# Kernel tuning notes

Measured on AMD Instinct MI355X. Metric: run time of the kernel, lower is better.

Reference implementation:

```python
import jax, jax.numpy as jnp
import numpy as np

IMG = 800.0        # image size (square)
STRIDE = 16        # backbone stride
PRE = 6000         # pre-NMS proposals (test_before_rpn_proposal_num)
POST = 300         # post-NMS proposals (test_after_rpn_proposal_num)
OUT = 7            # RoIAlign output size
SR = 2             # sampling ratio (fixed stand-in for adaptive -1)
NMS_THR = 0.7      # rpn_nms_thr_iou
MIN_SIZE = 16.0    # rpn_min_size
NCLS = 21          # num_classes + background
NEG = -1e30


def xywh2xyxy(b):
    return jnp.concatenate([b[..., :2], b[..., :2] + b[..., 2:]], -1)


def iou_one_vs_all(box, boxes):
    x1 = jnp.maximum(box[0], boxes[:, 0]); y1 = jnp.maximum(box[1], boxes[:, 1])
    x2 = jnp.minimum(box[2], boxes[:, 2]); y2 = jnp.minimum(box[3], boxes[:, 3])
    inter = jnp.maximum(x2 - x1, 0.0) * jnp.maximum(y2 - y1, 0.0)
    a = (box[2] - box[0]) * (box[3] - box[1])
    b = (boxes[:, 2] - boxes[:, 0]) * (boxes[:, 3] - boxes[:, 1])
    return inter / (a + b - inter + 1e-9)


def nms(boxes, scores, thr, k):
    # Greedy NMS with a fixed number of kept boxes (jit-static shapes).
    boxes = jax.lax.stop_gradient(boxes)
    scores = jax.lax.stop_gradient(scores)
    n = scores.shape[0]
    idx = jnp.arange(n)

    def step(sc, _):
        best = jnp.argmax(sc)
        ious = iou_one_vs_all(boxes[best], boxes)
        sc = jnp.where((ious > thr) | (idx == best), NEG, sc)
        return sc, best

    _, keep = jax.lax.scan(step, scores, None, length=k)
    return keep  # [k] int32 indices


def roi_align(feat, rois_xyxy, scale, out, sr):
    # feat [C,H,W], rois_xyxy [K,4] in image coords -> [K,C,out,out]
    C, H, W = feat.shape
    K = rois_xyxy.shape[0]
    x1 = rois_xyxy[:, 0] * scale; y1 = rois_xyxy[:, 1] * scale
    x2 = rois_xyxy[:, 2] * scale; y2 = rois_xyxy[:, 3] * scale
    bw = (x2 - x1) / out; bh = (y2 - y1) / out
    grid = jnp.arange(out, dtype=jnp.float32)
    sub = (jnp.arange(sr, dtype=jnp.float32) + 0.5) / sr
    xs = x1[:, None, None] + (grid[None, :, None] + sub[None, None, :]) * bw[:, None, None]  # [K,out,sr]
    ys = y1[:, None, None] + (grid[None, :, None] + sub[None, None, :]) * bh[:, None, None]
    shp = (K, out, out, sr, sr)  # [K, oy, ox, sy, sx]
    xg = jnp.broadcast_to(xs[:, None, :, None, :], shp)
    yg = jnp.broadcast_to(ys[:, :, None, :, None], shp)
    x0 = jnp.floor(xg); y0 = jnp.floor(yg)
    wx = xg - x0; wy = yg - y0
    x0i = jnp.clip(x0.astype(jnp.int32), 0, W - 1); x1i = jnp.clip(x0i + 1, 0, W - 1)
    y0i = jnp.clip(y0.astype(jnp.int32), 0, H - 1); y1i = jnp.clip(y0i + 1, 0, H - 1)
    v00 = feat[:, y0i, x0i]  # [C,K,out,out,sr,sr]
    v01 = feat[:, y0i, x1i]
    v10 = feat[:, y1i, x0i]
    v11 = feat[:, y1i, x1i]
    wx = wx[None]; wy = wy[None]
    val = v00 * (1 - wy) * (1 - wx) + v01 * (1 - wy) * wx + v10 * wy * (1 - wx) + v11 * wy * wx
    pooled = val.mean(axis=(-1, -2))  # [C,K,out,out]
    return jnp.transpose(pooled, (1, 0, 2, 3))


def _forward(feat, proposals, scores, fc1_w, fc1_b, fc2_w, fc2_b, cls_w, cls_b, reg_w, reg_b):
    std = jnp.tile(jnp.array([0.1, 0.1, 0.2, 0.2], jnp.float32), NCLS)  # target_std per class

    def per_image(fb, pr, sc):
        # mark small proposals as ignored (score -> -inf), as in forward
        sc = jnp.where((pr[:, 2] < MIN_SIZE) | (pr[:, 3] < MIN_SIZE), NEG, sc)
        tsc, tid = jax.lax.top_k(sc, PRE)
        tb = pr[tid]                       # [PRE,4] xywh
        txyxy = xywh2xyxy(tb)
        keep = nms(txyxy, tsc, NMS_THR, POST)
        sb = tb[keep]                      # [POST,4] xywh
        sxyxy = txyxy[keep]
        rf = roi_align(fb, sxyxy, 1.0 / STRIDE, OUT, SR)   # [POST,512,7,7]
        x = rf.reshape(POST, -1)
        x = jax.nn.relu(x @ fc1_w + fc1_b)
        x = jax.nn.relu(x @ fc2_w + fc2_b)
        cls = x @ cls_w + cls_b            # [POST,21]
        reg = (x @ reg_w + reg_b) * std    # reg * target_std + target_mean(=0)
        reg = reg.reshape(POST, NCLS, 4)
        # proposal2bbox: xy = p_xy + d_xy*p_wh ; wh = p_wh * exp(d_wh)
        xy = sb[:, None, :2] + reg[..., :2] * sb[:, None, 2:]
        wh = sb[:, None, 2:] * jnp.exp(reg[..., 2:])
        dec = jnp.clip(jnp.concatenate([xy, xy + wh], -1), 0.0, IMG)
        return jnp.concatenate([jax.nn.softmax(cls, -1), dec.reshape(POST, NCLS * 4)], -1)

    return jax.vmap(per_image)(feat, proposals, scores)  # [B, POST, 21 + 84]


def setup_inputs() -> dict:
    key = jax.random.key(0)
    ks = jax.random.split(key, 12)
    B, C, H, W = 1, 512, 50, 50
    N = 22500  # 50*50*9 anchors
    feat = jax.random.normal(ks[0], (B, C, H, W), jnp.float32)
    xy = jax.random.uniform(ks[1], (B, N, 2), jnp.float32) * (IMG - 64.0)
    wh = 8.0 + jax.random.uniform(ks[2], (B, N, 2), jnp.float32) * 392.0  # some below min_size=16
    proposals = jnp.concatenate([xy, wh], -1)
    scores = jax.random.uniform(ks[3], (B, N), jnp.float32)
    D = C * OUT * OUT  # 25088
    return {
        "feat": feat,
        "proposals": proposals,
        "scores": scores,
        "fc1_w": jax.random.normal(ks[4], (D, 4096), jnp.float32) * 0.01,
        "fc1_b": jnp.zeros((4096,), jnp.float32),
        "fc2_w": jax.random.normal(ks[5], (4096, 4096), jnp.float32) * 0.01,
        "fc2_b": jnp.zeros((4096,), jnp.float32),
        "cls_w": jax.random.normal(ks[6], (4096, NCLS), jnp.float32) * 0.01,
        "cls_b": jnp.zeros((NCLS,), jnp.float32),
        "reg_w": jax.random.normal(ks[7], (4096, NCLS * 4), jnp.float32) * 0.001,
        "reg_b": jnp.zeros((NCLS * 4,), jnp.float32),
    }


def reference(feat, proposals, scores, fc1_w, fc1_b, fc2_w, fc2_b, cls_w, cls_b, reg_w, reg_b):
    return _forward(feat, proposals, scores, fc1_w, fc1_b, fc2_w, fc2_b, cls_w, cls_b, reg_w, reg_b)
```

## Files before the change

### kernel.cpp

```cpp
#include <hip/hip_runtime.h>
#include <stdint.h>


#define NEGV -1e30f

typedef __attribute__((ext_vector_type(8))) short short8;
typedef __attribute__((ext_vector_type(4))) float f32x4;

__device__ __forceinline__ uint16_t f2bf(float f) {
  uint32_t u = __builtin_bit_cast(uint32_t, f);
  u = (u + 0x7FFFu + ((u >> 16) & 1u)) >> 16;
  return (uint16_t)u;
}
__device__ __forceinline__ float bf2f(uint16_t h) {
  return __builtin_bit_cast(float, ((uint32_t)h) << 16);
}
__device__ __forceinline__ uint32_t fkey(float f) {
  uint32_t u = __builtin_bit_cast(uint32_t, f);
  return (u & 0x80000000u) ? ~u : (u | 0x80000000u);
}

__global__ __launch_bounds__(256) void prep_kernel(
    const float* __restrict__ proposals, const float* __restrict__ scores,
    uint32_t* __restrict__ keys, uint64_t* __restrict__ sortbuf,
    int* __restrict__ counter) {
  int i = blockIdx.x * 256 + threadIdx.x;
  if (i < 8192) sortbuf[i] = 0ULL;
  if (i == 0) *counter = 0;
  if (i < 22500) {
    float w = proposals[i * 4 + 2], h = proposals[i * 4 + 3];
    float s = scores[i];
    s = (w < 16.0f || h < 16.0f) ? NEGV : s;
    keys[i] = fkey(s);
  }
}

__global__ __launch_bounds__(1024) void select_kernel(
    const uint32_t* __restrict__ keys, uint32_t* __restrict__ cutoff) {
  __shared__ uint32_t hist[256];
  __shared__ uint32_t s_prefix;
  __shared__ int s_remaining;
  int tid = threadIdx.x;
  if (tid == 0) { s_prefix = 0; s_remaining = 6000; }
  __syncthreads();
  for (int round = 0; round < 4; round++) {
    int shift = 24 - round * 8;
    for (int i = tid; i < 256; i += 1024) hist[i] = 0;
    __syncthreads();
    uint32_t prefix = s_prefix;
    uint32_t pmask = (round == 0) ? 0u : (0xFFFFFFFFu << (shift + 8));
    for (int i = tid; i < 22500; i += 1024) {
      uint32_t kv = keys[i];
      if ((kv & pmask) == (prefix & pmask))
        atomicAdd(&hist[(kv >> shift) & 255u], 1u);
    }
    __syncthreads();
    if (tid == 0) {
      int rem = s_remaining;
      int chosen = 0;
      for (int b = 255; b >= 0; b--) {
        int c = (int)hist[b];
        if (c >= rem) { chosen = b; break; }
        rem -= c;
      }
      s_prefix = prefix | ((uint32_t)chosen << shift);
      s_remaining = rem;
    }
    __syncthreads();
  }
  if (tid == 0) *cutoff = s_prefix;
}

__global__ __launch_bounds__(256) void compact_kernel(
    const uint32_t* __restrict__ keys, const uint32_t* __restrict__ cutoff,
    uint64_t* __restrict__ sortbuf, int* __restrict__ counter) {
  int i = blockIdx.x * 256 + threadIdx.x;
  if (i >= 22500) return;
  uint32_t kv = keys[i];
  if (kv >= *cutoff) {
    int p = atomicAdd(counter, 1);
    if (p < 8192)
      sortbuf[p] = ((uint64_t)kv << 32) | (uint32_t)(~(uint32_t)i);
  }
}

__global__ __launch_bounds__(1024) void sort_kernel(
    const uint64_t* __restrict__ sortbuf, int* __restrict__ sorted_idx) {
  __shared__ uint64_t v[8192];
  int tid = threadIdx.x;
  for (int i = tid; i < 8192; i += 1024) v[i] = sortbuf[i];
  __syncthreads();
  for (int k = 2; k <= 8192; k <<= 1) {
    for (int j = k >> 1; j > 0; j >>= 1) {
      for (int i = tid; i < 8192; i += 1024) {
        int ixj = i ^ j;
        if (ixj > i) {
          uint64_t a = v[i], b = v[ixj];
          bool up = (i & k) == 0;
          if (up ? (a < b) : (a > b)) { v[i] = b; v[ixj] = a; }
        }
      }
      __syncthreads();
    }
  }
  for (int i = tid; i < 6000; i += 1024)
    sorted_idx[i] = (int)(~(uint32_t)(v[i] & 0xFFFFFFFFull));
}

__global__ __launch_bounds__(256) void gather_kernel(
    const float* __restrict__ proposals, const int* __restrict__ sorted_idx,
    float4* __restrict__ sxyxy, float4* __restrict__ sxywh) {
  int i = blockIdx.x * 256 + threadIdx.x;
  if (i >= 6000) return;
  int oi = sorted_idx[i];
  float x = proposals[oi * 4 + 0], y = proposals[oi * 4 + 1];
  float w = proposals[oi * 4 + 2], h = proposals[oi * 4 + 3];
  sxywh[i] = make_float4(x, y, w, h);
  sxyxy[i] = make_float4(x, y, x + w, y + h);
}

__global__ __launch_bounds__(256) void ioumat_kernel(
    const float4* __restrict__ boxes, uint32_t* __restrict__ M) {
#pragma clang fp contract(off)
  int idx = blockIdx.x * 256 + threadIdx.x;
  if (idx >= 6000 * 188) return;
  int j = idx / 188;
  int w = idx - j * 188;
  float4 bb = boxes[j];
  float ba = (bb.z - bb.x) * (bb.w - bb.y);
  int base = w * 32;
  int lim = min(6000 - base, 32);
  uint32_t bits = 0;
  for (int b = 0; b < lim; b++) {
    float4 ob = boxes[base + b];
    float xx1 = fmaxf(bb.x, ob.x);
    float yy1 = fmaxf(bb.y, ob.y);
    float xx2 = fminf(bb.z, ob.z);
    float yy2 = fminf(bb.w, ob.w);
    float inter = fmaxf(xx2 - xx1, 0.0f) * fmaxf(yy2 - yy1, 0.0f);
    float oa = (ob.z - ob.x) * (ob.w - ob.y);
    float iou = inter / (ba + oa - inter + 1e-9f);
    if (iou > 0.7f) bits |= (1u << b);
  }
  M[idx] = bits;
}

__global__ __launch_bounds__(256) void nms_reduce_kernel(
    const uint32_t* __restrict__ M, const float4* __restrict__ sxyxy,
    const float4* __restrict__ sxywh, float4* __restrict__ keep_xyxy,
    float4* __restrict__ keep_xywh) {
  __shared__ uint32_t remv[188];
  __shared__ int keeps[300];
  __shared__ int s_ck[64];
  __shared__ int s_nk, s_nck;
  int tid = threadIdx.x;
  if (tid < 188) remv[tid] = (tid == 187) ? 0xFFFF0000u : 0u;
  if (tid == 0) { s_nk = 0; s_nck = 0; }
  __syncthreads();
  for (int c = 0; c < 94; c++) {
    if (tid < 64) {
      int row = c * 64 + tid;
      uint32_t lo = 0, hi = 0;
      if (row < 6000) {
        lo = M[(size_t)row * 188 + 2 * c];
        hi = M[(size_t)row * 188 + 2 * c + 1];
      }
      uint64_t alive =
          ~(((uint64_t)remv[2 * c + 1] << 32) | (uint64_t)remv[2 * c]);
      int nk = s_nk;
      int nck = 0;
      while (alive != 0 && nk < 300) {
        int b = (int)__builtin_ctzll(alive);
        int j = c * 64 + b;
        if (tid == 0) { keeps[nk] = j; s_ck[nck] = j; }
        nk++;
        nck++;
        uint64_t rb = ((uint64_t)(uint32_t)__shfl((int)hi, b, 64) << 32) |
                      (uint64_t)(uint32_t)__shfl((int)lo, b, 64);
        alive &= ~rb;
        alive &= ~(1ull << b);
      }
      if (tid == 0) { s_nk = nk; s_nck = nck; }
    }
    __syncthreads();
    int nck = s_nck;
    for (int kk = 0; kk < nck; kk++) {
      int j = s_ck[kk];
      if (tid < 188) remv[tid] |= M[(size_t)j * 188 + tid];
    }
    __syncthreads();
    if (s_nk >= 300) break;
  }
  __syncthreads();
  int nk = s_nk;
  for (int i = tid; i < 300; i += 256) {
    int kp = (i < nk) ? keeps[i] : 0;
    keep_xyxy[i] = sxyxy[kp];
    keep_xywh[i] = sxywh[kp];
  }
}

__global__ __launch_bounds__(256) void roi_kernel(
    const float* __restrict__ feat, const float4* __restrict__ keep_xyxy,
    uint16_t* __restrict__ A) {
  int r = blockIdx.x;
  int tid = threadIdx.x;
  uint16_t* out = A + (size_t)r * 25088;
  if (r >= 300) {
    for (int k = tid; k < 25088; k += 256) out[k] = 0;
    return;
  }
  __shared__ int xi0[14], xi1[14], yi0[14], yi1[14];
  __shared__ float wxs[14], wys[14];
  if (tid < 28) {
    int axis = tid / 14;
    int t = tid % 14;
    int g = t >> 1, sxi = t & 1;
    float4 box = keep_xyxy[r];
    float lo = (axis ? box.y : box.x) * 0.0625f;
    float hi = (axis ? box.w : box.z) * 0.0625f;
    float bsz = (hi - lo) / 7.0f;
    float sub = ((float)sxi + 0.5f) * 0.5f;
    float coord = lo + ((float)g + sub) * bsz;
    float f = floorf(coord);
    float frac = coord - f;
    int i0 = (int)f;
    i0 = min(max(i0, 0), 49);
    int i1 = min(i0 + 1, 49);
    if (axis == 0) { xi0[t] = i0; xi1[t] = i1; wxs[t] = frac; }
    else           { yi0[t] = i0; yi1[t] = i1; wys[t] = frac; }
  }
  __syncthreads();
  for (int k = tid; k < 25088; k += 256) {
    int c = k / 49;
    int pos = k - c * 49;
    int py = pos / 7, px = pos - py * 7;
    const float* fc = feat + (size_t)c * 2500;
    float val = 0.0f;
#pragma unroll
    for (int sy = 0; sy < 2; sy++) {
      int iy = py * 2 + sy;
      float wy = wys[iy];
      int y0 = yi0[iy], y1 = yi1[iy];
#pragma unroll
      for (int sx = 0; sx < 2; sx++) {
        int ix = px * 2 + sx;
        float wx = wxs[ix];
        int x0 = xi0[ix], x1 = xi1[ix];
        float v00 = fc[y0 * 50 + x0], v01 = fc[y0 * 50 + x1];
        float v10 = fc[y1 * 50 + x0], v11 = fc[y1 * 50 + x1];
        val += v00 * (1.0f - wy) * (1.0f - wx) + v01 * (1.0f - wy) * wx +
               v10 * wy * (1.0f - wx) + v11 * wy * wx;
      }
    }
    out[k] = f2bf(val * 0.25f);
  }
}

#define MTILES 5
#define NTILES 4
__global__ __launch_bounds__(256) void gemm_kernel(
    const uint16_t* __restrict__ A, const float* __restrict__ W,
    float* __restrict__ P, int K, int S) {
  __shared__ uint16_t As[320 * 32];
  __shared__ uint16_t Bs[64 * 40];
  const int nb = blockIdx.x;
  const int s = blockIdx.y;
  const int kchunk = K / S;
  const int steps = kchunk >> 5;
  const int k0base = s * kchunk;
  const int tid = threadIdx.x;
  const int w = tid >> 6;
  const int l = tid & 63;
  const int q = l >> 4;
  const int l15 = l & 15;

  f32x4 acc[MTILES][NTILES];
#pragma unroll
  for (int i = 0; i < MTILES; i++)
#pragma unroll
    for (int j = 0; j < NTILES; j++) acc[i][j] = (f32x4)0.0f;

  const int ng = (tid & 15) << 2;
  const int kp = tid >> 4;

  for (int kk = 0; kk < steps; kk++) {
    const int k0 = k0base + (kk << 5);
#pragma unroll
    for (int t = 0; t < 5; t++) {
      int cidx = w * 320 + t * 64 + l;
      int m = cidx >> 2;
      int co = (cidx & 3) << 3;
      const uint16_t* gp = A + (size_t)m * K + k0 + co;
      __builtin_amdgcn_global_load_lds(
          (const __attribute__((address_space(1))) void*)gp,
          (__attribute__((address_space(3))) void*)(As + (w * 320 + t * 64) * 8),
          16, 0, 0);
    }
    {
      const float* wp = W + (size_t)(k0 + 2 * kp) * 4096 + nb * 64 + ng;
      f32x4 f0 = *(const f32x4*)wp;
      f32x4 f1 = *(const f32x4*)(wp + 4096);
#pragma unroll
      for (int j = 0; j < 4; j++) {
        uint32_t v = (uint32_t)f2bf(f0[j]) | ((uint32_t)f2bf(f1[j]) << 16);
        *(uint32_t*)&Bs[(ng + j) * 40 + 2 * kp] = v;
      }
    }
    __syncthreads();
    short8 bfr[NTILES];
#pragma unroll
    for (int nt = 0; nt < NTILES; nt++)
      bfr[nt] = *(const short8*)&Bs[(nt * 16 + l15) * 40 + q * 8];
#pragma unroll
    for (int mt = 0; mt < MTILES; mt++) {
      int mrow = (w * MTILES + mt) * 16 + l15;
      short8 afr = *(const short8*)&As[mrow * 32 + q * 8];
#pragma unroll
      for (int nt = 0; nt < NTILES; nt++)
        acc[mt][nt] =
            __builtin_amdgcn_mfma_f32_16x16x32_bf16(afr, bfr[nt], acc[mt][nt], 0, 0, 0);
    }
    __syncthreads();
  }
#pragma unroll
  for (int mt = 0; mt < MTILES; mt++)
#pragma unroll
    for (int nt = 0; nt < NTILES; nt++)
#pragma unroll
      for (int r = 0; r < 4; r++) {
        int m = (w * MTILES + mt) * 16 + q * 4 + r;
        int n = nb * 64 + nt * 16 + l15;
        P[((size_t)s * 320 + m) * 4096 + n] = acc[mt][nt][r];
      }
}

__global__ __launch_bounds__(256) void reduce_kernel(
    const float* __restrict__ P, const float* __restrict__ bias,
    uint16_t* __restrict__ X) {
  int i = blockIdx.x * 256 + threadIdx.x;
  if (i >= 320 * 4096) return;
  int n = i & 4095;
  float s = 0.0f;
#pragma unroll
  for (int j = 0; j < 8; j++) s += P[(size_t)j * 320 * 4096 + i];
  s += bias[n];
  s = fmaxf(s, 0.0f);
  X[i] = f2bf(s);
}

__global__ __launch_bounds__(512) void head_kernel(
    const uint16_t* __restrict__ X3, const float* __restrict__ cls_w,
    const float* __restrict__ cls_b, const float* __restrict__ reg_w,
    const float* __restrict__ reg_b, const float4* __restrict__ keep_xywh,
    float* __restrict__ out) {
  int m = blockIdx.x;
  int tid = threadIdx.x;
  __shared__ float xr[4096];
  __shared__ float part[4][112];
  __shared__ float row[112];
  const uint16_t* xp = X3 + (size_t)m * 4096;
  for (int i = tid; i < 4096; i += 512) xr[i] = bf2f(xp[i]);
  __syncthreads();
  int qq = tid >> 7, n = tid & 127;
  if (n < 105) {
    float acc = 0.0f;
    int kbeg = qq * 1024;
    if (n < 21) {
      const float* wp = cls_w + n;
      for (int k = kbeg; k < kbeg + 1024; k++) acc += xr[k] * wp[k * 21];
    } else {
      const float* wp = reg_w + (n - 21);
      for (int k = kbeg; k < kbeg + 1024; k++) acc += xr[k] * wp[k * 84];
    }
    part[qq][n] = acc;
  }
  __syncthreads();
  if (tid < 105) {
    float v = part[0][tid] + part[1][tid] + part[2][tid] + part[3][tid];
    if (tid < 21) {
      v += cls_b[tid];
    } else {
      int j = tid - 21;
      v += reg_b[j];
      v *= ((j & 3) < 2) ? 0.1f : 0.2f;
    }
    row[tid] = v;
  }
  __syncthreads();
  if (tid < 105) {
    float val;
    if (tid < 21) {
      float mx = row[0];
      for (int j = 1; j < 21; j++) mx = fmaxf(mx, row[j]);
      float sum = 0.0f;
      for (int j = 0; j < 21; j++) sum += expf(row[j] - mx);
      val = expf(row[tid] - mx) / sum;
    } else {
      int j = tid - 21;
      int comp = j & 3;
      int cls = j >> 2;
      float r0 = row[21 + cls * 4 + 0];
      float r1 = row[21 + cls * 4 + 1];
      float r2 = row[21 + cls * 4 + 2];
      float r3 = row[21 + cls * 4 + 3];
      float4 sb = keep_xywh[m];
      float x = sb.x + r0 * sb.z;
      float y = sb.y + r1 * sb.w;
      if (comp == 0) val = x;
      else if (comp == 1) val = y;
      else if (comp == 2) val = x + sb.z * expf(r2);
      else val = y + sb.w * expf(r3);
      val = fminf(fmaxf(val, 0.0f), 800.0f);
    }
    out[(size_t)m * 105 + tid] = val;
  }
}

extern "C" void kernel_launch(void* const* d_in, const int* in_sizes, int n_in,
                              void* d_out, int out_size, void* d_ws, size_t ws_size,
                              hipStream_t stream) {
  const float* feat      = (const float*)d_in[0];
  const float* proposals = (const float*)d_in[1];
  const float* scores    = (const float*)d_in[2];
  const float* fc1_w     = (const float*)d_in[3];
  const float* fc1_b     = (const float*)d_in[4];
  const float* fc2_w     = (const float*)d_in[5];
  const float* fc2_b     = (const float*)d_in[6];
  const float* cls_w     = (const float*)d_in[7];
  const float* cls_b     = (const float*)d_in[8];
  const float* reg_w     = (const float*)d_in[9];
  const float* reg_b     = (const float*)d_in[10];
  float* out = (float*)d_out;

  char* ws = (char*)d_ws;
  size_t off = 0;
  auto alloc = [&](size_t bytes) -> void* {
    void* p = ws + off;
    off = (off + bytes + 255) & ~(size_t)255;
    return p;
  };
  uint32_t* keys      = (uint32_t*)alloc(22500 * 4);
  int*      misc      = (int*)alloc(256);
  uint64_t* sortbuf   = (uint64_t*)alloc(8192 * 8);
  int*      sorted_idx= (int*)alloc(6000 * 4);
  float4*   sxyxy     = (float4*)alloc(6000 * 16);
  float4*   sxywh     = (float4*)alloc(6000 * 16);
  float4*   keep_xyxy = (float4*)alloc(300 * 16);
  float4*   keep_xywh = (float4*)alloc(300 * 16);
  uint16_t* Abuf      = (uint16_t*)alloc((size_t)320 * 25088 * 2);
  uint16_t* X2        = (uint16_t*)alloc((size_t)320 * 4096 * 2);
  uint16_t* X3        = (uint16_t*)alloc((size_t)320 * 4096 * 2);
  float*    partials  = (float*)alloc((size_t)8 * 320 * 4096 * 4);
  uint32_t* cutoff    = (uint32_t*)misc;
  int*      counter   = misc + 1;
  uint32_t* M = (uint32_t*)partials;

  prep_kernel<<<88, 256, 0, stream>>>(proposals, scores, keys, sortbuf, counter);
  select_kernel<<<1, 1024, 0, stream>>>(keys, cutoff);
  compact_kernel<<<88, 256, 0, stream>>>(keys, cutoff, sortbuf, counter);
  sort_kernel<<<1, 1024, 0, stream>>>(sortbuf, sorted_idx);
  gather_kernel<<<24, 256, 0, stream>>>(proposals, sorted_idx, sxyxy, sxywh);
  ioumat_kernel<<<4407, 256, 0, stream>>>(sxyxy, M);
  nms_reduce_kernel<<<1, 256, 0, stream>>>(M, sxyxy, sxywh, keep_xyxy, keep_xywh);
  roi_kernel<<<320, 256, 0, stream>>>(feat, keep_xyxy, Abuf);
  gemm_kernel<<<dim3(64, 8), 256, 0, stream>>>(Abuf, fc1_w, partials, 25088, 8);
  reduce_kernel<<<5120, 256, 0, stream>>>(partials, fc1_b, X2);
  gemm_kernel<<<dim3(64, 8), 256, 0, stream>>>(X2, fc2_w, partials, 4096, 8);
  reduce_kernel<<<5120, 256, 0, stream>>>(partials, fc2_b, X3);
  head_kernel<<<300, 512, 0, stream>>>(X3, cls_w, cls_b, reg_w, reg_b, keep_xywh, out);
}
```

Measured before the change: 1.216 ms.

## Move classifier/regressor head onto MFMA GEMM and parallelize NMS mask OR

Replaces the per-RoI scalar head kernel, which re-read the strided cls/reg weights for every RoI, with three steps. A kernel converts and transposes the weights to bf16, a split-K MFMA GEMM over all RoIs writes partial sums, and a small epilogue reduces them and applies softmax and box decoding. Separately, the NMS suppression-mask update now spreads all newly kept rows across all threads using atomicOr instead of looping rows serially. The head now runs in bf16 instead of fp32, which may slightly change accuracy, and adds two extra launches plus partial-sum traffic.

```diff
diff --git a/kernel.cpp b/kernel.cpp
--- a/kernel.cpp
+++ b/kernel.cpp
@@ -184,9 +184,10 @@
     }
     __syncthreads();
     int nck = s_nck;
-    for (int kk = 0; kk < nck; kk++) {
-      int j = s_ck[kk];
-      if (tid < 188) remv[tid] |= M[(size_t)j * 188 + tid];
+    for (int i = tid; i < nck * 188; i += 256) {
+      int r = i / 188;
+      int wd = i - r * 188;
+      atomicOr(&remv[wd], M[(size_t)s_ck[r] * 188 + wd]);
     }
     __syncthreads();
     if (s_nk >= 300) break;
@@ -349,35 +350,70 @@
   X[i] = f2bf(s);
 }
 
-__global__ __launch_bounds__(512) void head_kernel(
-    const uint16_t* __restrict__ X3, const float* __restrict__ cls_w,
-    const float* __restrict__ cls_b, const float* __restrict__ reg_w,
+__global__ __launch_bounds__(256) void headw_kernel(
+    const float* __restrict__ cls_w, const float* __restrict__ reg_w,
+    uint16_t* __restrict__ Wh) {
+  int i = blockIdx.x * 256 + threadIdx.x;
+  if (i >= 112 * 4096) return;
+  int n = i >> 12, k = i & 4095;
+  float v = 0.0f;
+  if (n < 21) v = cls_w[k * 21 + n];
+  else if (n < 105) v = reg_w[k * 84 + (n - 21)];
+  Wh[i] = f2bf(v);
+}
+
+#define HNT 7
+__global__ __launch_bounds__(256) void headgemm_kernel(
+    const uint16_t* __restrict__ X3, const uint16_t* __restrict__ Wh,
+    float* __restrict__ HP) {
+  const int s = blockIdx.x;
+  const int tid = threadIdx.x;
+  const int w = tid >> 6, l = tid & 63, q = l >> 4, l15 = l & 15;
+  f32x4 acc[MTILES][HNT];
+#pragma unroll
+  for (int i = 0; i < MTILES; i++)
+#pragma unroll
+    for (int j = 0; j < HNT; j++) acc[i][j] = (f32x4)0.0f;
+#pragma unroll 4
+  for (int kk = 0; kk < 16; kk++) {
+    int k0 = s * 512 + kk * 32 + q * 8;
+    short8 bfr[HNT];
+#pragma unroll
+    for (int nt = 0; nt < HNT; nt++)
+      bfr[nt] = *(const short8*)(Wh + (size_t)(nt * 16 + l15) * 4096 + k0);
+#pragma unroll
+    for (int mt = 0; mt < MTILES; mt++) {
+      short8 afr =
+          *(const short8*)(X3 + (size_t)((w * MTILES + mt) * 16 + l15) * 4096 + k0);
+#pragma unroll
+      for (int nt = 0; nt < HNT; nt++)
+        acc[mt][nt] =
+            __builtin_amdgcn_mfma_f32_16x16x32_bf16(afr, bfr[nt], acc[mt][nt], 0, 0, 0);
+    }
+  }
+#pragma unroll
+  for (int mt = 0; mt < MTILES; mt++)
+#pragma unroll
+    for (int nt = 0; nt < HNT; nt++)
+#pragma unroll
+      for (int r = 0; r < 4; r++) {
+        int m = (w * MTILES + mt) * 16 + q * 4 + r;
+        int n = nt * 16 + l15;
+        HP[((size_t)s * 320 + m) * 112 + n] = acc[mt][nt][r];
+      }
+}
+
+__global__ __launch_bounds__(128) void head_epi_kernel(
+    const float* __restrict__ HP, const float* __restrict__ cls_b,
     const float* __restrict__ reg_b, const float4* __restrict__ keep_xywh,
     float* __restrict__ out) {
   int m = blockIdx.x;
   int tid = threadIdx.x;
-  __shared__ float xr[4096];
-  __shared__ float part[4][112];
   __shared__ float row[112];
-  const uint16_t* xp = X3 + (size_t)m * 4096;
-  for (int i = tid; i < 4096; i += 512) xr[i] = bf2f(xp[i]);
-  __syncthreads();
-  int qq = tid >> 7, n = tid & 127;
-  if (n < 105) {
-    float acc = 0.0f;
-    int kbeg = qq * 1024;
-    if (n < 21) {
-      const float* wp = cls_w + n;
-      for (int k = kbeg; k < kbeg + 1024; k++) acc += xr[k] * wp[k * 21];
-    } else {
-      const float* wp = reg_w + (n - 21);
-      for (int k = kbeg; k < kbeg + 1024; k++) acc += xr[k] * wp[k * 84];
-    }
-    part[qq][n] = acc;
-  }
-  __syncthreads();
   if (tid < 105) {
-    float v = part[0][tid] + part[1][tid] + part[2][tid] + part[3][tid];
+    float v = 0.0f;
+#pragma unroll
+    for (int s = 0; s < 8; s++) v += HP[((size_t)s * 320 + m) * 112 + tid];
     if (tid < 21) {
       v += cls_b[tid];
     } else {
@@ -451,6 +487,8 @@
   uint16_t* Abuf      = (uint16_t*)alloc((size_t)320 * 25088 * 2);
   uint16_t* X2        = (uint16_t*)alloc((size_t)320 * 4096 * 2);
   uint16_t* X3        = (uint16_t*)alloc((size_t)320 * 4096 * 2);
+  uint16_t* Wh        = (uint16_t*)alloc((size_t)112 * 4096 * 2);
+  float*    HP        = (float*)alloc((size_t)8 * 320 * 112 * 4);
   float*    partials  = (float*)alloc((size_t)8 * 320 * 4096 * 4);
   uint32_t* cutoff    = (uint32_t*)misc;
   int*      counter   = misc + 1;
@@ -464,9 +502,11 @@
   ioumat_kernel<<<4407, 256, 0, stream>>>(sxyxy, M);
   nms_reduce_kernel<<<1, 256, 0, stream>>>(M, sxyxy, sxywh, keep_xyxy, keep_xywh);
   roi_kernel<<<320, 256, 0, stream>>>(feat, keep_xyxy, Abuf);
+  headw_kernel<<<1792, 256, 0, stream>>>(cls_w, reg_w, Wh);
   gemm_kernel<<<dim3(64, 8), 256, 0, stream>>>(Abuf, fc1_w, partials, 25088, 8);
   reduce_kernel<<<5120, 256, 0, stream>>>(partials, fc1_b, X2);
   gemm_kernel<<<dim3(64, 8), 256, 0, stream>>>(X2, fc2_w, partials, 4096, 8);
   reduce_kernel<<<5120, 256, 0, stream>>>(partials, fc2_b, X3);
-  head_kernel<<<300, 512, 0, stream>>>(X3, cls_w, cls_b, reg_w, reg_b, keep_xywh, out);
-}
+  headgemm_kernel<<<8, 256, 0, stream>>>(X3, Wh, HP);
+  head_epi_kernel<<<300, 128, 0, stream>>>(HP, cls_b, reg_b, keep_xywh, out);
+}
```

New measurement: 1.216 ms. Within noise of the previous version (-0.0%).
